# Kernel optimization log

Measured on AMD Instinct MI355X. Metric: run time of the kernel, lower is better.

The kernel has to match this reference:

```python
import jax, jax.numpy as jnp
import numpy as np

# --- Config (Kimi/DeepSeek-style fine-grained MoE) ---
T = 4096        # num tokens
H = 1024        # hidden_size
I = 512         # moe_intermediate_size
E = 64          # num_experts
K = 8           # num_experts_per_token (top_k)
NG = 8          # num_expert_group
TKG = 4         # topk_group
NSH = 2         # num_shared_experts
IS = I * NSH    # shared-expert intermediate size
ROUTED_SCALE = 2.5


def setup_inputs() -> dict:
    key = jax.random.key(0)
    ks = jax.random.split(key, 7)
    s = 0.02
    return {
        "hidden_states": jax.random.normal(ks[0], (T, H), jnp.float32),
        "gate_w": jax.random.normal(ks[1], (E, H), jnp.float32) * s,          # router
        "e_bias": jax.random.normal(ks[2], (E,), jnp.float32) * 0.01,          # e_score_correction_bias
        "w1": jax.random.normal(ks[3], (E, H, 2 * I), jnp.float32) * s,       # per-expert gate_up
        "w2": jax.random.normal(ks[4], (E, I, H), jnp.float32) * s,           # per-expert down
        "sw_gu": jax.random.normal(ks[5], (H, 2 * IS), jnp.float32) * s,      # shared gate_up
        "sw_d": jax.random.normal(ks[6], (IS, H), jnp.float32) * s,           # shared down
    }


def _silu_and_mul(gu):
    d = gu.shape[-1] // 2
    return jax.nn.silu(gu[..., :d]) * gu[..., d:]


def _grouped_topk(scores, e_bias):
    """DeepSeek-V3/Kimi grouped top-k with sigmoid scoring + score-correction bias."""
    Tn = scores.shape[0]
    sfc = scores + e_bias[None, :]                       # scores_for_choice [T, E]
    # group score = sum of top-2 corrected scores inside each group
    grp = sfc.reshape(Tn, NG, E // NG)
    group_scores = jax.lax.top_k(grp, 2)[0].sum(-1)      # [T, NG]
    gidx = jax.lax.top_k(group_scores, TKG)[1]           # [T, TKG]
    gmask = jnp.zeros((Tn, NG), sfc.dtype).at[jnp.arange(Tn)[:, None], gidx].set(1.0)
    smask = jnp.repeat(gmask, E // NG, axis=1) > 0       # [T, E] bool
    tmp = jnp.where(smask, sfc, 0.0)                     # masked_fill(~mask, 0.0) as in vLLM
    topk_ids = jax.lax.top_k(tmp, K)[1]                  # [T, K]
    topk_w = jnp.take_along_axis(scores, topk_ids, axis=1)
    topk_w = topk_w / topk_w.sum(-1, keepdims=True)      # renormalize
    return topk_w, topk_ids


def _forward(x, gate_w, e_bias, w1, w2, sw_gu, sw_d):
    Tn, Hn = x.shape
    # shared experts (KimiMLP)
    shared = _silu_and_mul(x @ sw_gu) @ sw_d             # [T, H]
    # router
    logits = x @ gate_w.T                                # [T, E]
    scores = jax.nn.sigmoid(logits)
    topk_w, topk_ids = _grouped_topk(scores, e_bias)
    # dispatch: sort the T*K assignments by expert id -> grouped GEMM
    flat_ids = topk_ids.reshape(-1)                      # [T*K]
    order = jnp.argsort(flat_ids)                        # [T*K]
    tok = order // K                                     # token index of each sorted assignment
    xs = x[tok]                                          # [T*K, H] gathered tokens
    gsizes = jnp.bincount(flat_ids, length=E).astype(jnp.int32)
    gu = jax.lax.ragged_dot(xs, w1, gsizes)              # [T*K, 2I] grouped GEMM
    h = _silu_and_mul(gu)                                # [T*K, I]
    ys = jax.lax.ragged_dot(h, w2, gsizes)               # [T*K, H]
    # combine: scale by routing weight, scatter-add back to tokens
    flat_w = topk_w.reshape(-1)[order]                   # [T*K]
    routed = jnp.zeros((Tn, Hn), x.dtype).at[tok].add(ys * flat_w[:, None])
    return routed * ROUTED_SCALE + shared


def reference(hidden_states, gate_w, e_bias, w1, w2, sw_gu, sw_d):
    return _forward(hidden_states, gate_w, e_bias, w1, w2, sw_gu, sw_d)
```

## Files before the change

### kernel.cpp

```cpp
#include <hip/hip_runtime.h>
#include <cstdint>
#include <cstddef>

#define TT   4096
#define HH   1024
#define II   512
#define EE   64
#define KT   8
#define ISZ  1024
#define TKA  32768
#define MAXT 320

typedef __bf16 bf16x8 __attribute__((ext_vector_type(8)));
typedef float  f32x4  __attribute__((ext_vector_type(4)));
typedef unsigned short us8v __attribute__((ext_vector_type(8)));

__device__ __forceinline__ unsigned short f2bf(float f) {
  unsigned u = __float_as_uint(f);
  u += 0x7fffu + ((u >> 16) & 1u);
  return (unsigned short)(u >> 16);
}

#define GLDS(gp, lp) __builtin_amdgcn_global_load_lds( \
    (const __attribute__((address_space(1))) void*)(gp), \
    (__attribute__((address_space(3))) void*)(lp), 16, 0, 0)


__global__ __launch_bounds__(256) void k_transpose(const float* __restrict__ in,
                                                   unsigned short* __restrict__ out,
                                                   int R, int C) {
  __shared__ float tile[64][65];
  long b = blockIdx.z;
  int r0 = blockIdx.x * 64, c0 = blockIdx.y * 64;
  const float* ip = in + b * (long)R * C;
  unsigned short* op = out + b * (long)R * C;
  int tc = threadIdx.x & 63, tr = threadIdx.x >> 6;
#pragma unroll
  for (int rr = 0; rr < 64; rr += 4)
    tile[tr + rr][tc] = ip[(long)(r0 + tr + rr) * C + (c0 + tc)];
  __syncthreads();
#pragma unroll
  for (int rr = 0; rr < 64; rr += 4)
    op[(long)(c0 + tr + rr) * R + (r0 + tc)] = f2bf(tile[tc][tr + rr]);
}

__global__ __launch_bounds__(256) void k_cvt(const float* __restrict__ in,
                                             unsigned short* __restrict__ out) {
  int i = blockIdx.x * 256 + threadIdx.x;
  float4 v = ((const float4*)in)[i];
  ushort4 o;
  o.x = f2bf(v.x); o.y = f2bf(v.y); o.z = f2bf(v.z); o.w = f2bf(v.w);
  ((ushort4*)out)[i] = o;
}

__global__ __launch_bounds__(256) void k_router(const float* __restrict__ x,
    const float* __restrict__ gw, const float* __restrict__ eb,
    int* __restrict__ topk_ids, float* __restrict__ topk_w, int* __restrict__ counts)
{
  __shared__ float xrow[HH];
  __shared__ float sc[EE];
  int t = blockIdx.x;
  int tid = threadIdx.x;
  for (int i = tid; i < HH; i += 256) xrow[i] = x[(long)t * HH + i];
  __syncthreads();
  int e = tid >> 2, q = tid & 3;
  const float* w = gw + (long)e * HH;
  double acc = 0.0, acc2 = 0.0;
  for (int i = q * 8; i < HH; i += 32) {
    float4 wa = *(const float4*)(w + i);
    float4 wb = *(const float4*)(w + i + 4);
    acc  += (double)wa.x * (double)xrow[i]
          + (double)wa.y * (double)xrow[i + 1]
          + (double)wa.z * (double)xrow[i + 2]
          + (double)wa.w * (double)xrow[i + 3];
    acc2 += (double)wb.x * (double)xrow[i + 4]
          + (double)wb.y * (double)xrow[i + 5]
          + (double)wb.z * (double)xrow[i + 6]
          + (double)wb.w * (double)xrow[i + 7];
  }
  acc += acc2;
  acc += __shfl_down(acc, 2);
  acc += __shfl_down(acc, 1);
  if (q == 0) sc[e] = (float)(1.0 / (1.0 + exp(-acc)));
  __syncthreads();
  if (tid < 64) {
    int lane = tid;
    float s = sc[lane];
    float sfc = s + eb[lane];
    float m1 = sfc, m2 = -1e30f;
#pragma unroll
    for (int d = 1; d < 8; d <<= 1) {
      float o1 = __shfl_xor(m1, d);
      float o2 = __shfl_xor(m2, d);
      float hi = fmaxf(m1, o1);
      float lo = fminf(m1, o1);
      m2 = fmaxf(lo, fmaxf(m2, o2));
      m1 = hi;
    }
    float gs = m1 + m2;
    int g = lane >> 3;
    int grank = 0;
#pragma unroll
    for (int j = 0; j < 8; j++) {
      float gj = __shfl(gs, j * 8);
      if (gj > gs || (gj == gs && j < g)) grank++;
    }
    bool gsel = grank < 4;
    float mv = gsel ? sfc : 0.0f;
    int rank = 0;
    for (int j = 0; j < 64; j++) {
      float vj = __shfl(mv, j);
      if (vj > mv || (vj == mv && j < lane)) rank++;
    }
    bool sel = rank < KT;
    float ssum = sel ? s : 0.0f;
#pragma unroll
    for (int d = 1; d < 64; d <<= 1) ssum += __shfl_xor(ssum, d);
    unsigned long long bal = __ballot(sel);
    if (sel) {
      int pos = __popcll(bal & ((1ull << lane) - 1ull));
      topk_ids[(long)t * KT + pos] = lane;
      topk_w[(long)t * KT + pos] = s / ssum;
      atomicAdd(&counts[lane], 1);
    }
  }
}

__global__ void k_offsets(const int* __restrict__ counts, int* __restrict__ offsets,
                          int* __restrict__ cursor, int* __restrict__ tile_e,
                          int* __restrict__ tile_r0)
{
  int lane = threadIdx.x;
  int c = counts[lane];
  int xs = c;
#pragma unroll
  for (int d = 1; d < 64; d <<= 1) { int y = __shfl_up(xs, d); if (lane >= d) xs += y; }
  int off = xs - c;
  offsets[lane] = off;
  cursor[lane] = off;
  if (lane == 63) offsets[EE] = xs;
  int nt = (c + 127) >> 7;
  int tp = nt;
#pragma unroll
  for (int d = 1; d < 64; d <<= 1) { int y = __shfl_up(tp, d); if (lane >= d) tp += y; }
  int tbase = tp - nt;
  for (int i = 0; i < nt; i++) { tile_e[tbase + i] = lane; tile_r0[tbase + i] = off + i * 128; }
  int total = __shfl(tp, 63);
  for (int i = total + lane; i < MAXT; i += 64) tile_e[i] = -1;
}

__global__ __launch_bounds__(256) void k_scatter(const int* __restrict__ ids,
    const float* __restrict__ tw, int* __restrict__ cursor,
    int* __restrict__ perm, float* __restrict__ wslot, int* __restrict__ inv)
{
  int a = blockIdx.x * 256 + threadIdx.x;
  int e = ids[a];
  int pos = atomicAdd(&cursor[e], 1);
  perm[pos] = a >> 3;
  wslot[pos] = tw[a];
  inv[a] = pos;
}

__global__ __launch_bounds__(256) void k_gemm_gu(
    const unsigned short* __restrict__ Abase, const int* __restrict__ perm,
    const unsigned short* __restrict__ Bbase, long eStride, int Kd, int upOff,
    unsigned short* __restrict__ Hout,
    const int* __restrict__ tile_e, const int* __restrict__ tile_r0,
    const int* __restrict__ eoff, int rowsTotal)
{
  __shared__ __align__(16) unsigned short lds[8192];
  int e = 0, row0, end;
  if (tile_e) {
    e = tile_e[blockIdx.x];
    if (e < 0) return;
    row0 = tile_r0[blockIdx.x];
    end = eoff[e + 1];
  } else { row0 = blockIdx.x * 128; end = rowsTotal; }
  const unsigned short* B = Bbase + (long)e * eStride;
  int n0 = blockIdx.y * 64;
  int tid = threadIdx.x, lane = tid & 63, wave = tid >> 6;
  int wm = wave >> 1, wn = wave & 1;
  int lr = lane >> 2;
  int lkq = ((((lane & 3) - ((lane >> 3) & 3)) & 3)) * 8;
  int r0a = row0 + wave * 32 + lr;
  int r1a = r0a + 16;
  int t0 = r0a < rowsTotal ? r0a : rowsTotal - 1;
  int t1 = r1a < rowsTotal ? r1a : rowsTotal - 1;
  if (perm) { t0 = perm[t0]; t1 = perm[t1]; }
  const unsigned short* ap0 = Abase + (long)t0 * Kd + lkq;
  const unsigned short* ap1 = Abase + (long)t1 * Kd + lkq;
  const unsigned short* bg = B + (long)(n0 + wave * 16 + lr) * Kd + lkq;
  const unsigned short* bu = B + (long)(upOff + n0 + wave * 16 + lr) * Kd + lkq;
  unsigned short* lA0 = lds + wave * 1024 + lane * 8;
  unsigned short* lBg = lds + 4096 + wave * 512 + lane * 8;
  unsigned short* lBu = lds + 6144 + wave * 512 + lane * 8;
  f32x4 acc[4][4];
  f32x4 z = {0.f, 0.f, 0.f, 0.f};
  for (int i = 0; i < 4; i++) for (int j = 0; j < 4; j++) acc[i][j] = z;
  int quad = lane >> 4, cl = lane & 15;
  int sw8 = ((quad + ((cl >> 1) & 3)) & 3) * 8;
  for (int k0 = 0; k0 < Kd; k0 += 32) {
    __syncthreads();
    GLDS(ap0 + k0, lA0);
    GLDS(ap1 + k0, lA0 + 512);
    GLDS(bg + k0, lBg);
    GLDS(bu + k0, lBu);
    __syncthreads();
    bf16x8 af[4], bgf[2], buf2[2];
#pragma unroll
    for (int mi = 0; mi < 4; mi++)
      af[mi] = *(const bf16x8*)(lds + (wm * 64 + mi * 16 + cl) * 32 + sw8);
#pragma unroll
    for (int ni = 0; ni < 2; ni++) {
      bgf[ni]  = *(const bf16x8*)(lds + 4096 + (wn * 32 + ni * 16 + cl) * 32 + sw8);
      buf2[ni] = *(const bf16x8*)(lds + 6144 + (wn * 32 + ni * 16 + cl) * 32 + sw8);
    }
#pragma unroll
    for (int mi = 0; mi < 4; mi++) {
#pragma unroll
      for (int ni = 0; ni < 2; ni++) {
        acc[mi][ni]     = __builtin_amdgcn_mfma_f32_16x16x32_bf16(af[mi], bgf[ni],  acc[mi][ni],     0, 0, 0);
        acc[mi][ni + 2] = __builtin_amdgcn_mfma_f32_16x16x32_bf16(af[mi], buf2[ni], acc[mi][ni + 2], 0, 0, 0);
      }
    }
  }
#pragma unroll
  for (int mi = 0; mi < 4; mi++) {
#pragma unroll
    for (int j = 0; j < 2; j++) {
#pragma unroll
      for (int r = 0; r < 4; r++) {
        int row = row0 + wm * 64 + mi * 16 + quad * 4 + r;
        if (row < end) {
          float g = acc[mi][j][r], u = acc[mi][j + 2][r];
          float hv = g * (1.f / (1.f + __expf(-g))) * u;
          Hout[(long)row * upOff + (n0 + wn * 32 + j * 16 + cl)] = f2bf(hv);
        }
      }
    }
  }
}

__global__ __launch_bounds__(256) void k_gemm_down(
    const unsigned short* __restrict__ Abase,
    const unsigned short* __restrict__ Bbase, long eStride, int Kd,
    void* __restrict__ Outv, const float* __restrict__ wslot,
    const int* __restrict__ tile_e, const int* __restrict__ tile_r0,
    const int* __restrict__ eoff, int rowsTotal, int mode)
{
  __shared__ __align__(16) unsigned short lds[8192];
  int e = 0, row0, end;
  if (tile_e) {
    e = tile_e[blockIdx.x];
    if (e < 0) return;
    row0 = tile_r0[blockIdx.x];
    end = eoff[e + 1];
  } else { row0 = blockIdx.x * 128; end = rowsTotal; }
  const unsigned short* B = Bbase + (long)e * eStride;
  int n0 = blockIdx.y * 128;
  int tid = threadIdx.x, lane = tid & 63, wave = tid >> 6;
  int wm = wave >> 1, wn = wave & 1;
  int lr = lane >> 2;
  int lkq = ((((lane & 3) - ((lane >> 3) & 3)) & 3)) * 8;
  int r0a = row0 + wave * 32 + lr;
  int r1a = r0a + 16;
  int t0 = r0a < rowsTotal ? r0a : rowsTotal - 1;
  int t1 = r1a < rowsTotal ? r1a : rowsTotal - 1;
  const unsigned short* ap0 = Abase + (long)t0 * Kd + lkq;
  const unsigned short* ap1 = Abase + (long)t1 * Kd + lkq;
  const unsigned short* bp0 = B + (long)(n0 + wave * 32 + lr) * Kd + lkq;
  const unsigned short* bp1 = bp0 + (long)16 * Kd;
  unsigned short* lA0 = lds + wave * 1024 + lane * 8;
  unsigned short* lB0 = lds + 4096 + wave * 1024 + lane * 8;
  f32x4 acc[4][4];
  f32x4 z = {0.f, 0.f, 0.f, 0.f};
  for (int i = 0; i < 4; i++) for (int j = 0; j < 4; j++) acc[i][j] = z;
  int quad = lane >> 4, cl = lane & 15;
  int sw8 = ((quad + ((cl >> 1) & 3)) & 3) * 8;
  for (int k0 = 0; k0 < Kd; k0 += 32) {
    __syncthreads();
    GLDS(ap0 + k0, lA0);
    GLDS(ap1 + k0, lA0 + 512);
    GLDS(bp0 + k0, lB0);
    GLDS(bp1 + k0, lB0 + 512);
    __syncthreads();
    bf16x8 af[4], bfr[4];
#pragma unroll
    for (int mi = 0; mi < 4; mi++)
      af[mi] = *(const bf16x8*)(lds + (wm * 64 + mi * 16 + cl) * 32 + sw8);
#pragma unroll
    for (int ni = 0; ni < 4; ni++)
      bfr[ni] = *(const bf16x8*)(lds + 4096 + (wn * 64 + ni * 16 + cl) * 32 + sw8);
#pragma unroll
    for (int mi = 0; mi < 4; mi++)
#pragma unroll
      for (int ni = 0; ni < 4; ni++)
        acc[mi][ni] = __builtin_amdgcn_mfma_f32_16x16x32_bf16(af[mi], bfr[ni], acc[mi][ni], 0, 0, 0);
  }
#pragma unroll
  for (int mi = 0; mi < 4; mi++) {
    int rowb = row0 + wm * 64 + mi * 16 + quad * 4;
#pragma unroll
    for (int r = 0; r < 4; r++) {
      int row = rowb + r;
      if (row >= end) continue;
      if (mode) {
        unsigned short* Y = (unsigned short*)Outv;
        float scale = wslot[row] * 2.5f;
#pragma unroll
        for (int ni = 0; ni < 4; ni++) {
          int col = n0 + wn * 64 + ni * 16 + cl;
          Y[(long)row * HH + col] = f2bf(acc[mi][ni][r] * scale);
        }
      } else {
        float* O = (float*)Outv;
#pragma unroll
        for (int ni = 0; ni < 4; ni++) {
          int col = n0 + wn * 64 + ni * 16 + cl;
          O[(long)row * HH + col] = acc[mi][ni][r];
        }
      }
    }
  }
}

__global__ __launch_bounds__(256) void k_combine(const unsigned short* __restrict__ ys,
    const int* __restrict__ inv, float* __restrict__ out)
{
  int idx = blockIdx.x * 256 + threadIdx.x;
  int t = idx >> 7, c0 = (idx & 127) << 3;
  const int* ip = inv + (long)t * KT;
  float* op = out + (long)t * HH + c0;
  float4 o0 = *(float4*)op;
  float4 o1 = *(float4*)(op + 4);
  float a[8] = {o0.x, o0.y, o0.z, o0.w, o1.x, o1.y, o1.z, o1.w};
#pragma unroll
  for (int k = 0; k < KT; k++) {
    us8v v = *(const us8v*)(ys + (long)ip[k] * HH + c0);
#pragma unroll
    for (int j = 0; j < 8; j++) a[j] += __uint_as_float((unsigned)v[j] << 16);
  }
  *(float4*)op = make_float4(a[0], a[1], a[2], a[3]);
  *(float4*)(op + 4) = make_float4(a[4], a[5], a[6], a[7]);
}

extern "C" void kernel_launch(void* const* d_in, const int* in_sizes, int n_in,
                              void* d_out, int out_size, void* d_ws, size_t ws_size,
                              hipStream_t stream)
{
  const float* x   = (const float*)d_in[0];
  const float* gw  = (const float*)d_in[1];
  const float* eb  = (const float*)d_in[2];
  const float* w1  = (const float*)d_in[3];
  const float* w2  = (const float*)d_in[4];
  const float* sgu = (const float*)d_in[5];
  const float* sd  = (const float*)d_in[6];
  float* out = (float*)d_out;
  char* ws = (char*)d_ws;
  size_t off = 0;
  auto alloc = [&](size_t b) { void* p = ws + off; off += (b + 255) & ~(size_t)255; return p; };
  unsigned short* w1t  = (unsigned short*)alloc((size_t)EE * 2 * II * HH * 2);
  unsigned short* w2t  = (unsigned short*)alloc((size_t)EE * HH * II * 2);
  unsigned short* sgut = (unsigned short*)alloc((size_t)2 * ISZ * HH * 2);
  unsigned short* sdt  = (unsigned short*)alloc((size_t)HH * ISZ * 2);
  unsigned short* xb   = (unsigned short*)alloc((size_t)TT * HH * 2);
  unsigned short* hsb  = (unsigned short*)alloc((size_t)TT * ISZ * 2);
  unsigned short* hb   = (unsigned short*)alloc((size_t)TKA * II * 2);
  unsigned short* ys   = (unsigned short*)alloc((size_t)TKA * HH * 2);
  int*   tids   = (int*)alloc((size_t)TKA * 4);
  float* tw     = (float*)alloc((size_t)TKA * 4);
  int*   counts = (int*)alloc(256);
  int*   offs   = (int*)alloc(512);
  int*   cursor = (int*)alloc(256);
  int*   tile_e = (int*)alloc(MAXT * 4);
  int*   tile_r = (int*)alloc(MAXT * 4);
  int*   perm   = (int*)alloc((size_t)TKA * 4);
  float* wslot  = (float*)alloc((size_t)TKA * 4);
  int*   inv    = (int*)alloc((size_t)TKA * 4);

  hipMemsetAsync(counts, 0, 256, stream);
  dim3 b256(256);
  k_transpose<<<dim3(HH / 64, (2 * II) / 64, EE), b256, 0, stream>>>(w1, w1t, HH, 2 * II);
  k_transpose<<<dim3(II / 64, HH / 64, EE), b256, 0, stream>>>(w2, w2t, II, HH);
  k_transpose<<<dim3(HH / 64, (2 * ISZ) / 64, 1), b256, 0, stream>>>(sgu, sgut, HH, 2 * ISZ);
  k_transpose<<<dim3(ISZ / 64, HH / 64, 1), b256, 0, stream>>>(sd, sdt, ISZ, HH);
  k_cvt<<<dim3((TT * HH) / 1024), b256, 0, stream>>>(x, xb);
  k_router<<<dim3(TT), b256, 0, stream>>>(x, gw, eb, tids, tw, counts);
  k_offsets<<<dim3(1), dim3(64), 0, stream>>>(counts, offs, cursor, tile_e, tile_r);
  k_scatter<<<dim3(TKA / 256), b256, 0, stream>>>(tids, tw, cursor, perm, wslot, inv);
  k_gemm_gu<<<dim3(MAXT, II / 64), b256, 0, stream>>>(xb, perm, w1t, (long)2 * II * HH, HH, II,
                                                      hb, tile_e, tile_r, offs, TKA);
  k_gemm_down<<<dim3(MAXT, HH / 128), b256, 0, stream>>>(hb, w2t, (long)HH * II, II, (void*)ys,
                                                         wslot, tile_e, tile_r, offs, TKA, 1);
  k_gemm_gu<<<dim3(TT / 128, ISZ / 64), b256, 0, stream>>>(xb, nullptr, sgut, 0, HH, ISZ,
                                                           hsb, nullptr, nullptr, nullptr, TT);
  k_gemm_down<<<dim3(TT / 128, HH / 128), b256, 0, stream>>>(hsb, sdt, 0, ISZ, (void*)out,
                                                             nullptr, nullptr, nullptr, nullptr, TT, 0);
  k_combine<<<dim3(TT * 128 / 256), b256, 0, stream>>>(ys, inv, out);
}
```

Before: 969.6 us.

## Double-buffer LDS tiles in grouped GEMM kernels to overlap loads with MFMA

Both the gate-up and down GEMM kernels now use two LDS buffers. The global-to-LDS loads for the next K-slice are issued before the MFMAs on the current slice, and there is one barrier per iteration instead of two. The aim is to hide global load latency behind compute. LDS per block doubles to 32KB, which may reduce occupancy. The single barrier relies on the global_load_lds writes for the next slice having completed before the barrier, because no explicit vmcnt wait is shown.

New measurement: 939.8 us. 3.1% less time.

```diff
diff --git a/kernel.cpp b/kernel.cpp
--- a/kernel.cpp
+++ b/kernel.cpp
@@ -168,7 +168,7 @@
     const int* __restrict__ tile_e, const int* __restrict__ tile_r0,
     const int* __restrict__ eoff, int rowsTotal)
 {
-  __shared__ __align__(16) unsigned short lds[8192];
+  __shared__ __align__(16) unsigned short lds[16384];
   int e = 0, row0, end;
   if (tile_e) {
     e = tile_e[blockIdx.x];
@@ -199,21 +199,30 @@
   for (int i = 0; i < 4; i++) for (int j = 0; j < 4; j++) acc[i][j] = z;
   int quad = lane >> 4, cl = lane & 15;
   int sw8 = ((quad + ((cl >> 1) & 3)) & 3) * 8;
-  for (int k0 = 0; k0 < Kd; k0 += 32) {
-    __syncthreads();
-    GLDS(ap0 + k0, lA0);
-    GLDS(ap1 + k0, lA0 + 512);
-    GLDS(bg + k0, lBg);
-    GLDS(bu + k0, lBu);
-    __syncthreads();
+  GLDS(ap0, lA0);
+  GLDS(ap1, lA0 + 512);
+  GLDS(bg, lBg);
+  GLDS(bu, lBu);
+  __syncthreads();
+  int nk = Kd >> 5;
+  for (int t = 0; t < nk; ++t) {
+    int bo = (t & 1) << 13;
+    if (t + 1 < nk) {
+      int bo2 = 8192 - bo;
+      int k1 = (t + 1) << 5;
+      GLDS(ap0 + k1, lA0 + bo2);
+      GLDS(ap1 + k1, lA0 + bo2 + 512);
+      GLDS(bg + k1, lBg + bo2);
+      GLDS(bu + k1, lBu + bo2);
+    }
     bf16x8 af[4], bgf[2], buf2[2];
 #pragma unroll
     for (int mi = 0; mi < 4; mi++)
-      af[mi] = *(const bf16x8*)(lds + (wm * 64 + mi * 16 + cl) * 32 + sw8);
+      af[mi] = *(const bf16x8*)(lds + bo + (wm * 64 + mi * 16 + cl) * 32 + sw8);
 #pragma unroll
     for (int ni = 0; ni < 2; ni++) {
-      bgf[ni]  = *(const bf16x8*)(lds + 4096 + (wn * 32 + ni * 16 + cl) * 32 + sw8);
-      buf2[ni] = *(const bf16x8*)(lds + 6144 + (wn * 32 + ni * 16 + cl) * 32 + sw8);
+      bgf[ni]  = *(const bf16x8*)(lds + bo + 4096 + (wn * 32 + ni * 16 + cl) * 32 + sw8);
+      buf2[ni] = *(const bf16x8*)(lds + bo + 6144 + (wn * 32 + ni * 16 + cl) * 32 + sw8);
     }
 #pragma unroll
     for (int mi = 0; mi < 4; mi++) {
@@ -223,6 +232,7 @@
         acc[mi][ni + 2] = __builtin_amdgcn_mfma_f32_16x16x32_bf16(af[mi], buf2[ni], acc[mi][ni + 2], 0, 0, 0);
       }
     }
+    __syncthreads();
   }
 #pragma unroll
   for (int mi = 0; mi < 4; mi++) {
@@ -248,7 +258,7 @@
     const int* __restrict__ tile_e, const int* __restrict__ tile_r0,
     const int* __restrict__ eoff, int rowsTotal, int mode)
 {
-  __shared__ __align__(16) unsigned short lds[8192];
+  __shared__ __align__(16) unsigned short lds[16384];
   int e = 0, row0, end;
   if (tile_e) {
     e = tile_e[blockIdx.x];
@@ -277,25 +287,35 @@
   for (int i = 0; i < 4; i++) for (int j = 0; j < 4; j++) acc[i][j] = z;
   int quad = lane >> 4, cl = lane & 15;
   int sw8 = ((quad + ((cl >> 1) & 3)) & 3) * 8;
-  for (int k0 = 0; k0 < Kd; k0 += 32) {
-    __syncthreads();
-    GLDS(ap0 + k0, lA0);
-    GLDS(ap1 + k0, lA0 + 512);
-    GLDS(bp0 + k0, lB0);
-    GLDS(bp1 + k0, lB0 + 512);
-    __syncthreads();
+  GLDS(ap0, lA0);
+  GLDS(ap1, lA0 + 512);
+  GLDS(bp0, lB0);
+  GLDS(bp1, lB0 + 512);
+  __syncthreads();
+  int nk = Kd >> 5;
+  for (int t = 0; t < nk; ++t) {
+    int bo = (t & 1) << 13;
+    if (t + 1 < nk) {
+      int bo2 = 8192 - bo;
+      int k1 = (t + 1) << 5;
+      GLDS(ap0 + k1, lA0 + bo2);
+      GLDS(ap1 + k1, lA0 + bo2 + 512);
+      GLDS(bp0 + k1, lB0 + bo2);
+      GLDS(bp1 + k1, lB0 + bo2 + 512);
+    }
     bf16x8 af[4], bfr[4];
 #pragma unroll
     for (int mi = 0; mi < 4; mi++)
-      af[mi] = *(const bf16x8*)(lds + (wm * 64 + mi * 16 + cl) * 32 + sw8);
+      af[mi] = *(const bf16x8*)(lds + bo + (wm * 64 + mi * 16 + cl) * 32 + sw8);
 #pragma unroll
     for (int ni = 0; ni < 4; ni++)
-      bfr[ni] = *(const bf16x8*)(lds + 4096 + (wn * 64 + ni * 16 + cl) * 32 + sw8);
+      bfr[ni] = *(const bf16x8*)(lds + bo + 4096 + (wn * 64 + ni * 16 + cl) * 32 + sw8);
 #pragma unroll
     for (int mi = 0; mi < 4; mi++)
 #pragma unroll
       for (int ni = 0; ni < 4; ni++)
         acc[mi][ni] = __builtin_amdgcn_mfma_f32_16x16x32_bf16(af[mi], bfr[ni], acc[mi][ni], 0, 0, 0);
+    __syncthreads();
   }
 #pragma unroll
   for (int mi = 0; mi < 4; mi++) {
```

## Triple-buffer LDS tiles with async prefetch two steps ahead in MoE GEMMs

Applied to the files above, without the earlier changes.

Both grouped GEMM kernels (gate-up and down) now use a three-stage LDS ring buffer. Global-to-LDS loads for k-step t+2 are issued while step t is computed, and explicit vmcnt waits plus raw s_barrier replace the two __syncthreads per iteration. This is meant to hide global memory latency behind the MFMA work. LDS use triples to 48KB per block, which may lower occupancy, and the hand-counted vmcnt values must match the number of outstanding loads.

Measured after the change: 942.2 us. -2.8%, faster.

```diff
diff --git a/kernel.cpp b/kernel.cpp
--- a/kernel.cpp
+++ b/kernel.cpp
@@ -168,7 +168,7 @@
     const int* __restrict__ tile_e, const int* __restrict__ tile_r0,
     const int* __restrict__ eoff, int rowsTotal)
 {
-  __shared__ __align__(16) unsigned short lds[8192];
+  __shared__ __align__(16) unsigned short lds[24576];
   int e = 0, row0, end;
   if (tile_e) {
     e = tile_e[blockIdx.x];
@@ -199,21 +199,34 @@
   for (int i = 0; i < 4; i++) for (int j = 0; j < 4; j++) acc[i][j] = z;
   int quad = lane >> 4, cl = lane & 15;
   int sw8 = ((quad + ((cl >> 1) & 3)) & 3) * 8;
-  for (int k0 = 0; k0 < Kd; k0 += 32) {
-    __syncthreads();
-    GLDS(ap0 + k0, lA0);
-    GLDS(ap1 + k0, lA0 + 512);
-    GLDS(bg + k0, lBg);
-    GLDS(bu + k0, lBu);
-    __syncthreads();
+  int nk = Kd >> 5;
+  GLDS(ap0, lA0);            GLDS(ap1, lA0 + 512);
+  GLDS(bg,  lBg);            GLDS(bu,  lBu);
+  GLDS(ap0 + 32, lA0 + 8192); GLDS(ap1 + 32, lA0 + 8192 + 512);
+  GLDS(bg + 32,  lBg + 8192); GLDS(bu + 32,  lBu + 8192);
+  int cur = 0, nxt = 8192, fut = 16384;
+  for (int t = 0; t < nk; ++t) {
+    __builtin_amdgcn_s_barrier();
+    if (t + 2 < nk) {
+      int k2 = (t + 2) << 5;
+      GLDS(ap0 + k2, lA0 + fut); GLDS(ap1 + k2, lA0 + fut + 512);
+      GLDS(bg + k2,  lBg + fut); GLDS(bu + k2,  lBu + fut);
+      asm volatile("s_waitcnt vmcnt(8)" ::: "memory");
+    } else if (t + 1 < nk) {
+      asm volatile("s_waitcnt vmcnt(4)" ::: "memory");
+    } else {
+      asm volatile("s_waitcnt vmcnt(0)" ::: "memory");
+    }
+    __builtin_amdgcn_s_barrier();
+    asm volatile("" ::: "memory");
     bf16x8 af[4], bgf[2], buf2[2];
 #pragma unroll
     for (int mi = 0; mi < 4; mi++)
-      af[mi] = *(const bf16x8*)(lds + (wm * 64 + mi * 16 + cl) * 32 + sw8);
+      af[mi] = *(const bf16x8*)(lds + cur + (wm * 64 + mi * 16 + cl) * 32 + sw8);
 #pragma unroll
     for (int ni = 0; ni < 2; ni++) {
-      bgf[ni]  = *(const bf16x8*)(lds + 4096 + (wn * 32 + ni * 16 + cl) * 32 + sw8);
-      buf2[ni] = *(const bf16x8*)(lds + 6144 + (wn * 32 + ni * 16 + cl) * 32 + sw8);
+      bgf[ni]  = *(const bf16x8*)(lds + cur + 4096 + (wn * 32 + ni * 16 + cl) * 32 + sw8);
+      buf2[ni] = *(const bf16x8*)(lds + cur + 6144 + (wn * 32 + ni * 16 + cl) * 32 + sw8);
     }
 #pragma unroll
     for (int mi = 0; mi < 4; mi++) {
@@ -223,6 +236,8 @@
         acc[mi][ni + 2] = __builtin_amdgcn_mfma_f32_16x16x32_bf16(af[mi], buf2[ni], acc[mi][ni + 2], 0, 0, 0);
       }
     }
+    asm volatile("" ::: "memory");
+    int tmp = cur; cur = nxt; nxt = fut; fut = tmp;
   }
 #pragma unroll
   for (int mi = 0; mi < 4; mi++) {
@@ -248,7 +263,7 @@
     const int* __restrict__ tile_e, const int* __restrict__ tile_r0,
     const int* __restrict__ eoff, int rowsTotal, int mode)
 {
-  __shared__ __align__(16) unsigned short lds[8192];
+  __shared__ __align__(16) unsigned short lds[24576];
   int e = 0, row0, end;
   if (tile_e) {
     e = tile_e[blockIdx.x];
@@ -277,25 +292,40 @@
   for (int i = 0; i < 4; i++) for (int j = 0; j < 4; j++) acc[i][j] = z;
   int quad = lane >> 4, cl = lane & 15;
   int sw8 = ((quad + ((cl >> 1) & 3)) & 3) * 8;
-  for (int k0 = 0; k0 < Kd; k0 += 32) {
-    __syncthreads();
-    GLDS(ap0 + k0, lA0);
-    GLDS(ap1 + k0, lA0 + 512);
-    GLDS(bp0 + k0, lB0);
-    GLDS(bp1 + k0, lB0 + 512);
-    __syncthreads();
+  int nk = Kd >> 5;
+  GLDS(ap0, lA0);             GLDS(ap1, lA0 + 512);
+  GLDS(bp0, lB0);             GLDS(bp1, lB0 + 512);
+  GLDS(ap0 + 32, lA0 + 8192); GLDS(ap1 + 32, lA0 + 8192 + 512);
+  GLDS(bp0 + 32, lB0 + 8192); GLDS(bp1 + 32, lB0 + 8192 + 512);
+  int cur = 0, nxt = 8192, fut = 16384;
+  for (int t = 0; t < nk; ++t) {
+    __builtin_amdgcn_s_barrier();
+    if (t + 2 < nk) {
+      int k2 = (t + 2) << 5;
+      GLDS(ap0 + k2, lA0 + fut); GLDS(ap1 + k2, lA0 + fut + 512);
+      GLDS(bp0 + k2, lB0 + fut); GLDS(bp1 + k2, lB0 + fut + 512);
+      asm volatile("s_waitcnt vmcnt(8)" ::: "memory");
+    } else if (t + 1 < nk) {
+      asm volatile("s_waitcnt vmcnt(4)" ::: "memory");
+    } else {
+      asm volatile("s_waitcnt vmcnt(0)" ::: "memory");
+    }
+    __builtin_amdgcn_s_barrier();
+    asm volatile("" ::: "memory");
     bf16x8 af[4], bfr[4];
 #pragma unroll
     for (int mi = 0; mi < 4; mi++)
-      af[mi] = *(const bf16x8*)(lds + (wm * 64 + mi * 16 + cl) * 32 + sw8);
+      af[mi] = *(const bf16x8*)(lds + cur + (wm * 64 + mi * 16 + cl) * 32 + sw8);
 #pragma unroll
     for (int ni = 0; ni < 4; ni++)
-      bfr[ni] = *(const bf16x8*)(lds + 4096 + (wn * 64 + ni * 16 + cl) * 32 + sw8);
+      bfr[ni] = *(const bf16x8*)(lds + cur + 4096 + (wn * 64 + ni * 16 + cl) * 32 + sw8);
 #pragma unroll
     for (int mi = 0; mi < 4; mi++)
 #pragma unroll
       for (int ni = 0; ni < 4; ni++)
         acc[mi][ni] = __builtin_amdgcn_mfma_f32_16x16x32_bf16(af[mi], bfr[ni], acc[mi][ni], 0, 0, 0);
+    asm volatile("" ::: "memory");
+    int tmp = cur; cur = nxt; nxt = fut; fut = tmp;
   }
 #pragma unroll
   for (int mi = 0; mi < 4; mi++) {
```
